# Optimization experiments

Hardware: AMD Instinct MI355X
Metric: run time of the kernel (lower is better)

The kernel has to match this reference:

```python
import jax, jax.numpy as jnp
import numpy as np

N_WIN = 7  # winsize in PSF.forward
EMBED_DIM = 3
N_EMBED = 8192

def _box_sum(x, n=N_WIN):
    # sliding-window sum with zero padding == torch ZeroPad2d + unfold sum
    C = x.shape[1]
    k = jnp.ones((C, 1, n, n), x.dtype)
    return jax.lax.conv_general_dilated(
        x, k, (1, 1), [(n // 2, n // 2)] * 2,
        feature_group_count=C, dimension_numbers=('NCHW', 'OIHW', 'NCHW'))

def _patch_stats(x, n=N_WIN):
    # mean / unbiased var over the n*n window (zeros included, matching unfold of zero-padded input)
    N = n * n
    s1 = _box_sum(x, n)
    s2 = _box_sum(x * x, n)
    mean = s1 / N
    var = (s2 - s1 * s1 / N) / (N - 1)  # torch .var default unbiased=True
    return mean, var

def _patch_mv_norm(x, n=N_WIN):
    m, v = _patch_stats(x, n)
    return (x - m) / (jnp.sqrt(v) + 1e-8)

def _conv1x1(x, w, b):
    return jnp.einsum('oi,bihw->bohw', w, x) + b[None, :, None, None]

def _ln(x, g, b, eps=1e-5):
    m = x.mean(-1, keepdims=True)
    v = x.var(-1, keepdims=True)
    return (x - m) / jnp.sqrt(v + eps) * g + b

def _mlp(x, w1, b1, w2, b2):
    h = jax.nn.gelu(x @ w1.T + b1, approximate=True)  # GELU(approximate='tanh')
    return h @ w2.T + b2

def _psf(front, back, e_w, e_b, f_w, f_b, g_w, g_b, h_w, h_b):
    x_norm = _patch_mv_norm(front)
    y_mean, y_var = _patch_stats(back)
    x_adain = x_norm * jnp.sqrt(y_var) + y_mean  # patch_adain (no eps on y_std)
    EE = _conv1x1(x_adain, e_w, e_b)
    FF = _conv1x1(_patch_mv_norm(front), f_w, f_b)
    GG = _conv1x1(_patch_mv_norm(back), g_w, g_b)
    HH = _conv1x1(back, h_w, h_b)
    b, c, h, w = GG.shape
    FFf = FF.reshape(b, c, h * w)
    GGf = GG.reshape(b, c, h * w)
    F_n = jnp.sqrt((FFf * FFf).sum(1))
    G_n = jnp.sqrt((GGf * GGf).sum(1))
    S = (FFf * GGf).sum(1) / (F_n * G_n)          # [b, h*w] cosine similarity
    S_min = S.min(1, keepdims=True)
    S_max = S.max(1, keepdims=True)
    S_n = ((S - S_min) / (S_max - S_min)).reshape(b, 1, h, w)
    return S_n * EE + (1 - S_n) * HH

def reference(front, back, mask, bg_embed,
              mi_w1, mi_b1, mi_w2, mi_b2,
              q_w, k_w, v_w,
              mo_w1, mo_b1, mo_w2, mo_b2,
              n1_g, n1_b, n2_g, n2_b,
              e_w, e_b, f_w, f_b, g_w, g_b, h_w, h_b,
              fuse_w, fuse_b):
    fused = _psf(front, back, e_w, e_b, f_w, f_b, g_w, g_b, h_w, h_b)  # [B,3,H,W]
    B, C, H, W = front.shape
    x = front.reshape(B, C, H * W).transpose(0, 2, 1)   # [B, HW, 3] pixel tokens
    x = _mlp(x, mi_w1, mi_b1, mi_w2, mi_b2)             # mlp_in: 3 -> 6 -> embed_dim
    x = _ln(x, n1_g, n1_b)                              # norm1
    ctx = bg_embed.T                                    # [n_embed, embed_dim] codebook as context
    q = x @ q_w.T                                       # [B, HW, d]
    k = ctx @ k_w.T                                     # [n_embed, d]
    v = ctx @ v_w.T                                     # [n_embed, d]
    scale = q.shape[-1] ** (-0.5)
    attn = jax.nn.softmax(jnp.einsum('bld,nd->bln', q, k) * scale, axis=-1)
    x = jnp.einsum('bln,nd->bld', attn, v)              # [B, HW, d]
    x = _mlp(x, mo_w1, mo_b1, mo_w2, mo_b2)             # mlp_out: d -> 6 -> 3
    x = _ln(x, n2_g, n2_b)                              # norm2
    attn_img = x.transpose(0, 2, 1).reshape(B, 3, H, W)
    out = _conv1x1(jnp.concatenate([attn_img, fused], 1), fuse_w, fuse_b)  # fuse: 6 -> 3
    return out

def setup_inputs() -> dict:
    key = jax.random.key(0)
    ks = jax.random.split(key, 32)
    B, H, W = 2, 96, 96
    d = EMBED_DIM
    n = lambda k, s: jax.random.normal(k, s, dtype=jnp.float32)
    inp = {
        'front': n(ks[0], (B, 3, H, W)),
        'back':  n(ks[1], (B, 3, H, W)),
        'mask':  jax.random.uniform(ks[2], (B, 1, H, W), dtype=jnp.float32),
        'bg_embed': n(ks[3], (d, N_EMBED)),
        'mi_w1': n(ks[4], (6, 3)) * 0.5, 'mi_b1': jnp.zeros((6,)),
        'mi_w2': n(ks[5], (d, 6)) * 0.5, 'mi_b2': jnp.zeros((d,)),
        'q_w': n(ks[6], (d, d)) * 0.5,
        'k_w': n(ks[7], (d, d)) * 0.5,
        'v_w': n(ks[8], (d, d)) * 0.5,
        'mo_w1': n(ks[9], (6, d)) * 0.5, 'mo_b1': jnp.zeros((6,)),
        'mo_w2': n(ks[10], (3, 6)) * 0.5, 'mo_b2': jnp.zeros((3,)),
        'n1_g': jnp.ones((d,)), 'n1_b': jnp.zeros((d,)),
        'n2_g': jnp.ones((3,)), 'n2_b': jnp.zeros((3,)),
        'e_w': n(ks[11], (3, 3)) * 0.3, 'e_b': jnp.zeros((3,)),
        'f_w': n(ks[12], (3, 3)) * 0.3, 'f_b': jnp.zeros((3,)),
        'g_w': n(ks[13], (3, 3)) * 0.3, 'g_b': jnp.zeros((3,)),
        'h_w': n(ks[14], (3, 3)) * 0.3, 'h_b': jnp.zeros((3,)),
        'fuse_w': n(ks[15], (3, 6)) * 0.3, 'fuse_b': jnp.zeros((3,)),
    }
    return inp
```

## Files before the change

kernel.cpp:

```cpp
#include <hip/hip_runtime.h>
#include <math.h>

#define HW    9216
#define NPIX  18432
#define NKEY  8192

#define OFF_QPK  0
#define OFF_KPK  (OFF_QPK + NPIX*8)
#define OFF_VT   (OFF_KPK + NKEY*8)
#define OFF_EEHS (OFF_VT + NKEY*4)
#define OFF_MM   (OFF_EEHS + NPIX*8)
#define OFF_PART (OFF_MM + 576)

#if __has_builtin(__builtin_amdgcn_exp2f)
#define EXP2(x) __builtin_amdgcn_exp2f(x)
#else
#define EXP2(x) exp2f(x)
#endif

typedef float f32x4 __attribute__((ext_vector_type(4)));
typedef short bf16x8 __attribute__((ext_vector_type(8)));
typedef unsigned u32x4 __attribute__((ext_vector_type(4)));

__device__ __forceinline__ unsigned bf16rne(float x){
    unsigned b = __builtin_bit_cast(unsigned, x);
    return (b + 0x7FFFu + ((b >> 16) & 1u)) >> 16;
}
__device__ __forceinline__ float bf16tof(unsigned h){
    return __builtin_bit_cast(float, h << 16);
}

__device__ __forceinline__ float gelu_tanh(float x){
    float u = 0.7978845608028654f*(x + 0.044715f*x*x*x);
    return 0.5f*x*(1.0f + tanhf(u));
}

__global__ __launch_bounds__(256) void k1_prep(
    const float* __restrict__ front, const float* __restrict__ back,
    const float* __restrict__ bg,
    const float* __restrict__ k_w,  const float* __restrict__ v_w,
    const float* __restrict__ mi_w1, const float* __restrict__ mi_b1,
    const float* __restrict__ mi_w2, const float* __restrict__ mi_b2,
    const float* __restrict__ q_w,
    const float* __restrict__ n1_g, const float* __restrict__ n1_b,
    const float* __restrict__ e_w,  const float* __restrict__ e_b,
    const float* __restrict__ f_w,  const float* __restrict__ f_b,
    const float* __restrict__ g_w,  const float* __restrict__ g_b,
    const float* __restrict__ h_w,  const float* __restrict__ h_b,
    float* __restrict__ ws)
{
    float* ws_qpk  = ws + OFF_QPK;
    float* ws_kpk  = ws + OFF_KPK;
    float* ws_eehs = ws + OFF_EEHS;
    float* ws_mm   = ws + OFF_MM;

    __shared__ float lds[6][484];

    int tid = threadIdx.x;
    int bid = blockIdx.x;
    int img = bid / 36;
    int t   = bid % 36;
    int ty  = (t / 6) * 16;
    int tx  = (t % 6) * 16;

    if (bid < 32){
        int key = bid*256 + tid;
        float c0=bg[key], c1=bg[NKEY+key], c2=bg[2*NKEY+key];
        float kv3[3], vv3[3];
        #pragma unroll
        for (int i=0;i<3;i++){
            kv3[i] = k_w[i*3+0]*c0 + k_w[i*3+1]*c1 + k_w[i*3+2]*c2;
            vv3[i] = v_w[i*3+0]*c0 + v_w[i*3+1]*c1 + v_w[i*3+2]*c2;
        }
        unsigned kh[3], kl[3];
        #pragma unroll
        for (int i=0;i<3;i++){
            kh[i] = bf16rne(kv3[i]);
            kl[i] = bf16rne(kv3[i] - bf16tof(kh[i]));
        }
        unsigned u[8];
        u[0] = kh[0] | (kh[1]<<16);
        u[1] = kh[2] | (kl[0]<<16);
        u[2] = kl[1] | (kl[2]<<16);
        u[3] = kh[0] | (kh[1]<<16);
        u[4] = kh[2]; u[5]=0; u[6]=0; u[7]=0;
        f32x4* kp4 = (f32x4*)ws_kpk;
        kp4[(size_t)key*2+0] = __builtin_bit_cast(f32x4, *(const u32x4*)&u[0]);
        kp4[(size_t)key*2+1] = __builtin_bit_cast(f32x4, *(const u32x4*)&u[4]);
        ((f32x4*)(ws + OFF_VT))[key] = (f32x4){vv3[0], vv3[1], vv3[2], 0.0f};
    }

    const float* fbase = front + img*3*HW;
    const float* bbase = back  + img*3*HW;

    for (int i = tid; i < 484; i += 256){
        int hy = i / 22, hx = i - hy*22;
        int gy = ty + hy - 3, gx = tx + hx - 3;
        bool ok = ((unsigned)gy < 96u) && ((unsigned)gx < 96u);
        int off = gy*96 + gx;
        #pragma unroll
        for (int c=0;c<3;c++){
            lds[c  ][i] = ok ? fbase[c*HW+off] : 0.0f;
            lds[3+c][i] = ok ? bbase[c*HW+off] : 0.0f;
        }
    }
    __syncthreads();

    int ly = tid / 16, lx = tid - ly*16;
    int y  = ty + ly,  x  = tx + lx;
    int pos = y*96 + x;
    int pix = img*HW + pos;

    float s1f[3]={0,0,0}, s2f[3]={0,0,0}, s1b[3]={0,0,0}, s2b[3]={0,0,0};
    #pragma unroll
    for (int dy=0; dy<7; ++dy){
        int rb = (ly+dy)*22 + lx;
        #pragma unroll
        for (int dx=0; dx<7; ++dx){
            #pragma unroll
            for (int c=0;c<3;c++){
                float fv = lds[c  ][rb+dx];
                float bv = lds[3+c][rb+dx];
                s1f[c]+=fv; s2f[c]+=fv*fv;
                s1b[c]+=bv; s2b[c]+=bv*bv;
            }
        }
    }

    int ctr = (ly+3)*22 + (lx+3);
    float xnf[3], adain[3], bn[3], bval[3], fctr[3];
    #pragma unroll
    for (int c=0;c<3;c++){
        float mf = s1f[c]*(1.0f/49.0f);
        float vf = (s2f[c] - s1f[c]*s1f[c]*(1.0f/49.0f))*(1.0f/48.0f);
        float fv = lds[c][ctr];
        fctr[c] = fv;
        xnf[c] = (fv - mf)/(sqrtf(vf)+1e-8f);

        float mb = s1b[c]*(1.0f/49.0f);
        float vb = (s2b[c] - s1b[c]*s1b[c]*(1.0f/49.0f))*(1.0f/48.0f);
        float bb = lds[3+c][ctr];
        bval[c]  = bb;
        float stdb = sqrtf(vb);
        adain[c] = xnf[c]*stdb + mb;
        bn[c]    = (bb - mb)/(stdb + 1e-8f);
    }

    float EE[3], FF[3], GG[3], HHv[3];
    #pragma unroll
    for (int i=0;i<3;i++){
        EE[i]  = e_w[i*3+0]*adain[0] + e_w[i*3+1]*adain[1] + e_w[i*3+2]*adain[2] + e_b[i];
        FF[i]  = f_w[i*3+0]*xnf[0]   + f_w[i*3+1]*xnf[1]   + f_w[i*3+2]*xnf[2]   + f_b[i];
        GG[i]  = g_w[i*3+0]*bn[0]    + g_w[i*3+1]*bn[1]    + g_w[i*3+2]*bn[2]    + g_b[i];
        HHv[i] = h_w[i*3+0]*bval[0]  + h_w[i*3+1]*bval[1]  + h_w[i*3+2]*bval[2]  + h_b[i];
    }
    float num = FF[0]*GG[0]+FF[1]*GG[1]+FF[2]*GG[2];
    float fn  = sqrtf(FF[0]*FF[0]+FF[1]*FF[1]+FF[2]*FF[2]);
    float gn  = sqrtf(GG[0]*GG[0]+GG[1]*GG[1]+GG[2]*GG[2]);
    float S   = num/(fn*gn);

    float4* eehs4 = (float4*)ws_eehs;
    eehs4[pix*2+0] = make_float4(EE[0],EE[1],EE[2],S);
    eehs4[pix*2+1] = make_float4(HHv[0],HHv[1],HHv[2],0.0f);

    float mn = S, mx = S;
    #pragma unroll
    for (int off=32; off>0; off>>=1){
        mn = fminf(mn, __shfl_xor(mn, off));
        mx = fmaxf(mx, __shfl_xor(mx, off));
    }
    if ((tid & 63) == 0){
        int entry = bid*4 + (tid>>6);
        ws_mm[entry*2+0]=mn; ws_mm[entry*2+1]=mx;
    }

    float xt0 = fctr[0], xt1 = fctr[1], xt2 = fctr[2];
    float h6[6];
    #pragma unroll
    for (int i=0;i<6;i++){
        float a = mi_w1[i*3+0]*xt0 + mi_w1[i*3+1]*xt1 + mi_w1[i*3+2]*xt2 + mi_b1[i];
        h6[i] = gelu_tanh(a);
    }
    float x2[3];
    #pragma unroll
    for (int i=0;i<3;i++){
        float a = mi_b2[i];
        #pragma unroll
        for (int k=0;k<6;k++) a += mi_w2[i*6+k]*h6[k];
        x2[i]=a;
    }
    float m  = (x2[0]+x2[1]+x2[2])*(1.0f/3.0f);
    float d0 = x2[0]-m, d1 = x2[1]-m, d2 = x2[2]-m;
    float var = (d0*d0+d1*d1+d2*d2)*(1.0f/3.0f);
    float inv = 1.0f/sqrtf(var+1e-5f);
    float xn0 = d0*inv*n1_g[0]+n1_b[0];
    float xn1 = d1*inv*n1_g[1]+n1_b[1];
    float xn2 = d2*inv*n1_g[2]+n1_b[2];
    const float qs = 0.5773502691896258f * 1.4426950408889634f;
    float qv[3];
    qv[0] = (q_w[0]*xn0 + q_w[1]*xn1 + q_w[2]*xn2)*qs;
    qv[1] = (q_w[3]*xn0 + q_w[4]*xn1 + q_w[5]*xn2)*qs;
    qv[2] = (q_w[6]*xn0 + q_w[7]*xn1 + q_w[8]*xn2)*qs;

    unsigned qh[3], ql[3];
    #pragma unroll
    for (int i=0;i<3;i++){
        qh[i] = bf16rne(qv[i]);
        ql[i] = bf16rne(qv[i] - bf16tof(qh[i]));
    }
    unsigned u[8];
    u[0] = qh[0] | (qh[1]<<16);
    u[1] = qh[2] | (qh[0]<<16);
    u[2] = qh[1] | (qh[2]<<16);
    u[3] = ql[0] | (ql[1]<<16);
    u[4] = ql[2]; u[5]=0; u[6]=0; u[7]=0;
    f32x4* qp4 = (f32x4*)ws_qpk;
    qp4[(size_t)pix*2+0] = __builtin_bit_cast(f32x4, *(const u32x4*)&u[0]);
    qp4[(size_t)pix*2+1] = __builtin_bit_cast(f32x4, *(const u32x4*)&u[4]);
}

#define RED4(vv, mm) { vv.x += __shfl_xor(vv.x,mm); vv.y += __shfl_xor(vv.y,mm); \
                       vv.z += __shfl_xor(vv.z,mm); vv.w += __shfl_xor(vv.w,mm); }

__global__ __launch_bounds__(256) void k2_attn(const float* __restrict__ ws)
{
    const f32x4* qpk = (const f32x4*)(ws + OFF_QPK);
    const f32x4* kpk = (const f32x4*)(ws + OFF_KPK);
    const f32x4* vt  = (const f32x4*)(ws + OFF_VT);
    f32x4* part      = (f32x4*)(ws + OFF_PART);

    __shared__ f32x4 lkp[512];
    __shared__ f32x4 lv[256];

    int tid  = threadIdx.x;
    int bid  = blockIdx.x;
    int kq   = bid & 7;
    int qg   = bid >> 3;
    int wave = tid >> 6, lane = tid & 63;
    int qtile = qg*4 + wave;
    int g = lane >> 4, col = lane & 15;

    bf16x8 afrag = {0,0,0,0,0,0,0,0};
    if (g < 2)
        afrag = __builtin_bit_cast(bf16x8, qpk[(size_t)(qtile*16 + col)*2 + g]);

    f32x4 s_ = {0,0,0,0}, a0_ = {0,0,0,0}, a1_ = {0,0,0,0}, a2_ = {0,0,0,0};

    const f32x4* kpbase = kpk + ((size_t)kq*1024)*2;
    const f32x4* vbase  = vt + kq*1024;

    for (int chunk=0; chunk<4; ++chunk){
        for (int i=tid; i<512; i+=256) lkp[i] = kpbase[chunk*512 + i];
        if (tid < 256)             lv[tid] = vbase[chunk*256 + tid];
        __syncthreads();
        #pragma unroll 4
        for (int st=0; st<16; ++st){
            bf16x8 bfrag = {0,0,0,0,0,0,0,0};
            if (g < 2)
                bfrag = __builtin_bit_cast(bf16x8, lkp[(st*16+col)*2 + g]);
            f32x4 S = __builtin_amdgcn_mfma_f32_16x16x32_bf16(afrag, bfrag, (f32x4){0,0,0,0}, 0, 0, 0);
            f32x4 v = lv[st*16+col];
            f32x4 p;
            p.x = EXP2(S.x); p.y = EXP2(S.y); p.z = EXP2(S.z); p.w = EXP2(S.w);
            s_  += p;
            a0_ += p * v.x;
            a1_ += p * v.y;
            a2_ += p * v.z;
        }
        __syncthreads();
    }

    RED4(s_, 8) RED4(a0_, 8) RED4(a1_, 8) RED4(a2_, 8)
    RED4(s_, 4) RED4(a0_, 4) RED4(a1_, 4) RED4(a2_, 4)
    RED4(s_, 2) RED4(a0_, 2) RED4(a1_, 2) RED4(a2_, 2)
    RED4(s_, 1) RED4(a0_, 1) RED4(a1_, 1) RED4(a2_, 1)

    int qbase = qtile*16 + g*4;
    f32x4* dst = part + (size_t)kq*NPIX + qbase;
    if      (col==0) dst[0] = (f32x4){s_.x, a0_.x, a1_.x, a2_.x};
    else if (col==1) dst[1] = (f32x4){s_.y, a0_.y, a1_.y, a2_.y};
    else if (col==2) dst[2] = (f32x4){s_.z, a0_.z, a1_.z, a2_.z};
    else if (col==3) dst[3] = (f32x4){s_.w, a0_.w, a1_.w, a2_.w};
}

template<int NC_T>
__global__ __launch_bounds__(256) void k3_final(
    const float* __restrict__ ws,
    const float* __restrict__ mo_w1, const float* __restrict__ mo_b1,
    const float* __restrict__ mo_w2, const float* __restrict__ mo_b2,
    const float* __restrict__ n2_g,  const float* __restrict__ n2_b,
    const float* __restrict__ fuse_w,const float* __restrict__ fuse_b,
    float* __restrict__ out)
{
    const float* ws_eehs = ws + OFF_EEHS;
    const float* ws_mm   = ws + OFF_MM;
    const float* ws_part = ws + OFF_PART;

    int tid = threadIdx.x;
    int g   = tid >> 6;
    int lp  = tid & 63;
    int pixbase = blockIdx.x*64;
    int pix = pixbase + lp;
    int b   = (pix >= HW) ? 1 : 0;

    constexpr int CPG = NC_T/4;
    float s=0.0f, a0=0.0f, a1=0.0f, a2=0.0f;
    const f32x4* part4 = (const f32x4*)ws_part;
    #pragma unroll
    for (int c=g*CPG; c<(g+1)*CPG; ++c){
        f32x4 p = part4[(size_t)c*NPIX + pix];
        s+=p.x; a0+=p.y; a1+=p.z; a2+=p.w;
    }
    __shared__ f32x4 red[256];
    red[tid] = (f32x4){s,a0,a1,a2};

    __shared__ float wmn[4], wmx[4];
    float mn = INFINITY, mx = -INFINITY;
    if (tid < 144){
        mn = ws_mm[(b*144+tid)*2+0];
        mx = ws_mm[(b*144+tid)*2+1];
    }
    #pragma unroll
    for (int off=32; off>0; off>>=1){
        mn = fminf(mn, __shfl_xor(mn, off));
        mx = fmaxf(mx, __shfl_xor(mx, off));
    }
    if ((tid & 63) == 0){ wmn[tid>>6]=mn; wmx[tid>>6]=mx; }
    __syncthreads();

    if (tid < 64){
        mn = fminf(fminf(wmn[0],wmn[1]), fminf(wmn[2],wmn[3]));
        mx = fmaxf(fmaxf(wmx[0],wmx[1]), fmaxf(wmx[2],wmx[3]));

        f32x4 p0 = red[tid], p1 = red[64+tid], p2 = red[128+tid], p3 = red[192+tid];
        s  = p0.x+p1.x+p2.x+p3.x;
        a0 = p0.y+p1.y+p2.y+p3.y;
        a1 = p0.z+p1.z+p2.z+p3.z;
        a2 = p0.w+p1.w+p2.w+p3.w;
        float invs = 1.0f/s;
        float xa0 = a0*invs, xa1 = a1*invs, xa2 = a2*invs;

        float h6[6];
        #pragma unroll
        for (int i=0;i<6;i++){
            float a = mo_w1[i*3+0]*xa0 + mo_w1[i*3+1]*xa1 + mo_w1[i*3+2]*xa2 + mo_b1[i];
            h6[i] = gelu_tanh(a);
        }
        float y[3];
        #pragma unroll
        for (int i=0;i<3;i++){
            float a = mo_b2[i];
            #pragma unroll
            for (int k=0;k<6;k++) a += mo_w2[i*6+k]*h6[k];
            y[i]=a;
        }
        float m  = (y[0]+y[1]+y[2])*(1.0f/3.0f);
        float d0 = y[0]-m, d1 = y[1]-m, d2 = y[2]-m;
        float var = (d0*d0+d1*d1+d2*d2)*(1.0f/3.0f);
        float inv = 1.0f/sqrtf(var+1e-5f);
        float t0 = d0*inv*n2_g[0]+n2_b[0];
        float t1 = d1*inv*n2_g[1]+n2_b[1];
        float t2 = d2*inv*n2_g[2]+n2_b[2];

        float4 e  = ((const float4*)ws_eehs)[pix*2+0];
        float4 hh = ((const float4*)ws_eehs)[pix*2+1];
        float Sn = (e.w - mn)/(mx - mn);
        float f0 = Sn*e.x + (1.0f-Sn)*hh.x;
        float f1 = Sn*e.y + (1.0f-Sn)*hh.y;
        float f2 = Sn*e.z + (1.0f-Sn)*hh.z;

        int pos = pix - b*HW;
        #pragma unroll
        for (int o=0;o<3;o++){
            float val = fuse_b[o]
                      + fuse_w[o*6+0]*t0 + fuse_w[o*6+1]*t1 + fuse_w[o*6+2]*t2
                      + fuse_w[o*6+3]*f0 + fuse_w[o*6+4]*f1 + fuse_w[o*6+5]*f2;
            out[(b*3+o)*HW + pos] = val;
        }
    }
}

extern "C" void kernel_launch(void* const* d_in, const int* in_sizes, int n_in,
                              void* d_out, int out_size, void* d_ws, size_t ws_size,
                              hipStream_t stream) {
    const float* front  = (const float*)d_in[0];
    const float* back   = (const float*)d_in[1];
    const float* bg     = (const float*)d_in[3];
    const float* mi_w1  = (const float*)d_in[4];
    const float* mi_b1  = (const float*)d_in[5];
    const float* mi_w2  = (const float*)d_in[6];
    const float* mi_b2  = (const float*)d_in[7];
    const float* q_w    = (const float*)d_in[8];
    const float* k_w    = (const float*)d_in[9];
    const float* v_w    = (const float*)d_in[10];
    const float* mo_w1  = (const float*)d_in[11];
    const float* mo_b1  = (const float*)d_in[12];
    const float* mo_w2  = (const float*)d_in[13];
    const float* mo_b2  = (const float*)d_in[14];
    const float* n1_g   = (const float*)d_in[15];
    const float* n1_b   = (const float*)d_in[16];
    const float* n2_g   = (const float*)d_in[17];
    const float* n2_b   = (const float*)d_in[18];
    const float* e_w    = (const float*)d_in[19];
    const float* e_b    = (const float*)d_in[20];
    const float* f_w    = (const float*)d_in[21];
    const float* f_b    = (const float*)d_in[22];
    const float* g_w    = (const float*)d_in[23];
    const float* g_b    = (const float*)d_in[24];
    const float* h_w    = (const float*)d_in[25];
    const float* h_b    = (const float*)d_in[26];
    const float* fuse_w = (const float*)d_in[27];
    const float* fuse_b = (const float*)d_in[28];

    float* ws  = (float*)d_ws;
    float* out = (float*)d_out;

    k1_prep<<<dim3(72), 256, 0, stream>>>(
        front, back, bg, k_w, v_w, mi_w1, mi_b1, mi_w2, mi_b2, q_w,
        n1_g, n1_b, e_w, e_b, f_w, f_b, g_w, g_b, h_w, h_b, ws);

    k2_attn<<<dim3(2304), 256, 0, stream>>>(ws);

    k3_final<8><<<dim3(NPIX/64), 256, 0, stream>>>(
        ws, mo_w1, mo_b1, mo_w2, mo_b2, n2_g, n2_b, fuse_w, fuse_b, out);
}
```

Before: 52.73 us.

## Split prep kernel into smaller tiles with 4 threads per pixel

The prep kernel now uses 8x8 pixel tiles over 288 blocks instead of 16x16 tiles over 72 blocks, so far more of the GPU's compute units get work. Each pixel's 7x7 window sums are split by rows across four waves, and the partial sums are combined through shared memory before one wave finishes the per-pixel math. The aim is to shorten this under-parallelised stage. The cost is an extra barrier, a larger shared-memory reduction buffer, more halo loads per pixel, and three of four waves sitting idle during the epilogue.

```diff
diff --git a/kernel.cpp b/kernel.cpp
--- a/kernel.cpp
+++ b/kernel.cpp
@@ -54,14 +54,15 @@
     float* ws_eehs = ws + OFF_EEHS;
     float* ws_mm   = ws + OFF_MM;
 
-    __shared__ float lds[6][484];
+    __shared__ float lds[6][196];
+    __shared__ float red[12][256];
 
     int tid = threadIdx.x;
     int bid = blockIdx.x;
-    int img = bid / 36;
-    int t   = bid % 36;
-    int ty  = (t / 6) * 16;
-    int tx  = (t % 6) * 16;
+    int img = bid / 144;
+    int t   = bid % 144;
+    int ty  = (t / 12) * 8;
+    int tx  = (t % 12) * 8;
 
     if (bid < 32){
         int key = bid*256 + tid;
@@ -93,8 +94,8 @@
     const float* fbase = front + img*3*HW;
     const float* bbase = back  + img*3*HW;
 
-    for (int i = tid; i < 484; i += 256){
-        int hy = i / 22, hx = i - hy*22;
+    for (int i = tid; i < 196; i += 256){
+        int hy = i / 14, hx = i - hy*14;
         int gy = ty + hy - 3, gx = tx + hx - 3;
         bool ok = ((unsigned)gy < 96u) && ((unsigned)gx < 96u);
         int off = gy*96 + gx;
@@ -106,117 +107,142 @@
     }
     __syncthreads();
 
-    int ly = tid / 16, lx = tid - ly*16;
-    int y  = ty + ly,  x  = tx + lx;
-    int pos = y*96 + x;
-    int pix = img*HW + pos;
-
-    float s1f[3]={0,0,0}, s2f[3]={0,0,0}, s1b[3]={0,0,0}, s2b[3]={0,0,0};
-    #pragma unroll
-    for (int dy=0; dy<7; ++dy){
-        int rb = (ly+dy)*22 + lx;
-        #pragma unroll
-        for (int dx=0; dx<7; ++dx){
+    int p  = tid & 63;
+    int qd = tid >> 6;
+    int ly = p >> 3, lx = p & 7;
+
+    {
+        float s1f[3]={0,0,0}, s2f[3]={0,0,0}, s1b[3]={0,0,0}, s2b[3]={0,0,0};
+        int r0 = qd*2;
+        int nr = (qd < 3) ? 2 : 1;
+        for (int rr=0; rr<nr; ++rr){
+            int rb = (ly + r0 + rr)*14 + lx;
+            #pragma unroll
+            for (int dx=0; dx<7; ++dx){
+                #pragma unroll
+                for (int c=0;c<3;c++){
+                    float fv = lds[c  ][rb+dx];
+                    float bv = lds[3+c][rb+dx];
+                    s1f[c]+=fv; s2f[c]+=fv*fv;
+                    s1b[c]+=bv; s2b[c]+=bv*bv;
+                }
+            }
+        }
+        #pragma unroll
+        for (int c=0;c<3;c++){
+            red[c  ][tid] = s1f[c];
+            red[3+c][tid] = s2f[c];
+            red[6+c][tid] = s1b[c];
+            red[9+c][tid] = s2b[c];
+        }
+    }
+    __syncthreads();
+
+    if (tid < 64){
+        float s1f[3]={0,0,0}, s2f[3]={0,0,0}, s1b[3]={0,0,0}, s2b[3]={0,0,0};
+        #pragma unroll
+        for (int q2=0; q2<4; ++q2){
+            int src = p + q2*64;
             #pragma unroll
             for (int c=0;c<3;c++){
-                float fv = lds[c  ][rb+dx];
-                float bv = lds[3+c][rb+dx];
-                s1f[c]+=fv; s2f[c]+=fv*fv;
-                s1b[c]+=bv; s2b[c]+=bv*bv;
+                s1f[c] += red[c  ][src];
+                s2f[c] += red[3+c][src];
+                s1b[c] += red[6+c][src];
+                s2b[c] += red[9+c][src];
             }
         }
-    }
-
-    int ctr = (ly+3)*22 + (lx+3);
-    float xnf[3], adain[3], bn[3], bval[3], fctr[3];
-    #pragma unroll
-    for (int c=0;c<3;c++){
-        float mf = s1f[c]*(1.0f/49.0f);
-        float vf = (s2f[c] - s1f[c]*s1f[c]*(1.0f/49.0f))*(1.0f/48.0f);
-        float fv = lds[c][ctr];
-        fctr[c] = fv;
-        xnf[c] = (fv - mf)/(sqrtf(vf)+1e-8f);
-
-        float mb = s1b[c]*(1.0f/49.0f);
-        float vb = (s2b[c] - s1b[c]*s1b[c]*(1.0f/49.0f))*(1.0f/48.0f);
-        float bb = lds[3+c][ctr];
-        bval[c]  = bb;
-        float stdb = sqrtf(vb);
-        adain[c] = xnf[c]*stdb + mb;
-        bn[c]    = (bb - mb)/(stdb + 1e-8f);
-    }
-
-    float EE[3], FF[3], GG[3], HHv[3];
-    #pragma unroll
-    for (int i=0;i<3;i++){
-        EE[i]  = e_w[i*3+0]*adain[0] + e_w[i*3+1]*adain[1] + e_w[i*3+2]*adain[2] + e_b[i];
-        FF[i]  = f_w[i*3+0]*xnf[0]   + f_w[i*3+1]*xnf[1]   + f_w[i*3+2]*xnf[2]   + f_b[i];
-        GG[i]  = g_w[i*3+0]*bn[0]    + g_w[i*3+1]*bn[1]    + g_w[i*3+2]*bn[2]    + g_b[i];
-        HHv[i] = h_w[i*3+0]*bval[0]  + h_w[i*3+1]*bval[1]  + h_w[i*3+2]*bval[2]  + h_b[i];
-    }
-    float num = FF[0]*GG[0]+FF[1]*GG[1]+FF[2]*GG[2];
-    float fn  = sqrtf(FF[0]*FF[0]+FF[1]*FF[1]+FF[2]*FF[2]);
-    float gn  = sqrtf(GG[0]*GG[0]+GG[1]*GG[1]+GG[2]*GG[2]);
-    float S   = num/(fn*gn);
-
-    float4* eehs4 = (float4*)ws_eehs;
-    eehs4[pix*2+0] = make_float4(EE[0],EE[1],EE[2],S);
-    eehs4[pix*2+1] = make_float4(HHv[0],HHv[1],HHv[2],0.0f);
-
-    float mn = S, mx = S;
-    #pragma unroll
-    for (int off=32; off>0; off>>=1){
-        mn = fminf(mn, __shfl_xor(mn, off));
-        mx = fmaxf(mx, __shfl_xor(mx, off));
-    }
-    if ((tid & 63) == 0){
-        int entry = bid*4 + (tid>>6);
-        ws_mm[entry*2+0]=mn; ws_mm[entry*2+1]=mx;
-    }
-
-    float xt0 = fctr[0], xt1 = fctr[1], xt2 = fctr[2];
-    float h6[6];
-    #pragma unroll
-    for (int i=0;i<6;i++){
-        float a = mi_w1[i*3+0]*xt0 + mi_w1[i*3+1]*xt1 + mi_w1[i*3+2]*xt2 + mi_b1[i];
-        h6[i] = gelu_tanh(a);
-    }
-    float x2[3];
-    #pragma unroll
-    for (int i=0;i<3;i++){
-        float a = mi_b2[i];
-        #pragma unroll
-        for (int k=0;k<6;k++) a += mi_w2[i*6+k]*h6[k];
-        x2[i]=a;
-    }
-    float m  = (x2[0]+x2[1]+x2[2])*(1.0f/3.0f);
-    float d0 = x2[0]-m, d1 = x2[1]-m, d2 = x2[2]-m;
-    float var = (d0*d0+d1*d1+d2*d2)*(1.0f/3.0f);
-    float inv = 1.0f/sqrtf(var+1e-5f);
-    float xn0 = d0*inv*n1_g[0]+n1_b[0];
-    float xn1 = d1*inv*n1_g[1]+n1_b[1];
-    float xn2 = d2*inv*n1_g[2]+n1_b[2];
-    const float qs = 0.5773502691896258f * 1.4426950408889634f;
-    float qv[3];
-    qv[0] = (q_w[0]*xn0 + q_w[1]*xn1 + q_w[2]*xn2)*qs;
-    qv[1] = (q_w[3]*xn0 + q_w[4]*xn1 + q_w[5]*xn2)*qs;
-    qv[2] = (q_w[6]*xn0 + q_w[7]*xn1 + q_w[8]*xn2)*qs;
-
-    unsigned qh[3], ql[3];
-    #pragma unroll
-    for (int i=0;i<3;i++){
-        qh[i] = bf16rne(qv[i]);
-        ql[i] = bf16rne(qv[i] - bf16tof(qh[i]));
-    }
-    unsigned u[8];
-    u[0] = qh[0] | (qh[1]<<16);
-    u[1] = qh[2] | (qh[0]<<16);
-    u[2] = qh[1] | (qh[2]<<16);
-    u[3] = ql[0] | (ql[1]<<16);
-    u[4] = ql[2]; u[5]=0; u[6]=0; u[7]=0;
-    f32x4* qp4 = (f32x4*)ws_qpk;
-    qp4[(size_t)pix*2+0] = __builtin_bit_cast(f32x4, *(const u32x4*)&u[0]);
-    qp4[(size_t)pix*2+1] = __builtin_bit_cast(f32x4, *(const u32x4*)&u[4]);
+
+        int ctr = (ly+3)*14 + (lx+3);
+        int pos = (ty+ly)*96 + (tx+lx);
+        int pix = img*HW + pos;
+
+        float xnf[3], adain[3], bn[3], bval[3], fctr[3];
+        #pragma unroll
+        for (int c=0;c<3;c++){
+            float mf = s1f[c]*(1.0f/49.0f);
+            float vf = (s2f[c] - s1f[c]*s1f[c]*(1.0f/49.0f))*(1.0f/48.0f);
+            float fv = lds[c][ctr];
+            fctr[c] = fv;
+            xnf[c] = (fv - mf)/(sqrtf(vf)+1e-8f);
+
+            float mb = s1b[c]*(1.0f/49.0f);
+            float vb = (s2b[c] - s1b[c]*s1b[c]*(1.0f/49.0f))*(1.0f/48.0f);
+            float bb = lds[3+c][ctr];
+            bval[c]  = bb;
+            float stdb = sqrtf(vb);
+            adain[c] = xnf[c]*stdb + mb;
+            bn[c]    = (bb - mb)/(stdb + 1e-8f);
+        }
+
+        float EE[3], FF[3], GG[3], HHv[3];
+        #pragma unroll
+        for (int i=0;i<3;i++){
+            EE[i]  = e_w[i*3+0]*adain[0] + e_w[i*3+1]*adain[1] + e_w[i*3+2]*adain[2] + e_b[i];
+            FF[i]  = f_w[i*3+0]*xnf[0]   + f_w[i*3+1]*xnf[1]   + f_w[i*3+2]*xnf[2]   + f_b[i];
+            GG[i]  = g_w[i*3+0]*bn[0]    + g_w[i*3+1]*bn[1]    + g_w[i*3+2]*bn[2]    + g_b[i];
+            HHv[i] = h_w[i*3+0]*bval[0]  + h_w[i*3+1]*bval[1]  + h_w[i*3+2]*bval[2]  + h_b[i];
+        }
+        float num = FF[0]*GG[0]+FF[1]*GG[1]+FF[2]*GG[2];
+        float fn  = sqrtf(FF[0]*FF[0]+FF[1]*FF[1]+FF[2]*FF[2]);
+        float gn  = sqrtf(GG[0]*GG[0]+GG[1]*GG[1]+GG[2]*GG[2]);
+        float S   = num/(fn*gn);
+
+        float4* eehs4 = (float4*)ws_eehs;
+        eehs4[pix*2+0] = make_float4(EE[0],EE[1],EE[2],S);
+        eehs4[pix*2+1] = make_float4(HHv[0],HHv[1],HHv[2],0.0f);
+
+        float mn = S, mx = S;
+        #pragma unroll
+        for (int off=32; off>0; off>>=1){
+            mn = fminf(mn, __shfl_xor(mn, off));
+            mx = fmaxf(mx, __shfl_xor(mx, off));
+        }
+        if (p == 0){ ws_mm[bid*2+0]=mn; ws_mm[bid*2+1]=mx; }
+
+        float xt0 = fctr[0], xt1 = fctr[1], xt2 = fctr[2];
+        float h6[6];
+        #pragma unroll
+        for (int i=0;i<6;i++){
+            float a = mi_w1[i*3+0]*xt0 + mi_w1[i*3+1]*xt1 + mi_w1[i*3+2]*xt2 + mi_b1[i];
+            h6[i] = gelu_tanh(a);
+        }
+        float x2[3];
+        #pragma unroll
+        for (int i=0;i<3;i++){
+            float a = mi_b2[i];
+            #pragma unroll
+            for (int k=0;k<6;k++) a += mi_w2[i*6+k]*h6[k];
+            x2[i]=a;
+        }
+        float m  = (x2[0]+x2[1]+x2[2])*(1.0f/3.0f);
+        float d0 = x2[0]-m, d1 = x2[1]-m, d2 = x2[2]-m;
+        float var = (d0*d0+d1*d1+d2*d2)*(1.0f/3.0f);
+        float inv = 1.0f/sqrtf(var+1e-5f);
+        float xn0 = d0*inv*n1_g[0]+n1_b[0];
+        float xn1 = d1*inv*n1_g[1]+n1_b[1];
+        float xn2 = d2*inv*n1_g[2]+n1_b[2];
+        const float qs = 0.5773502691896258f * 1.4426950408889634f;
+        float qv[3];
+        qv[0] = (q_w[0]*xn0 + q_w[1]*xn1 + q_w[2]*xn2)*qs;
+        qv[1] = (q_w[3]*xn0 + q_w[4]*xn1 + q_w[5]*xn2)*qs;
+        qv[2] = (q_w[6]*xn0 + q_w[7]*xn1 + q_w[8]*xn2)*qs;
+
+        unsigned qh[3], ql[3];
+        #pragma unroll
+        for (int i=0;i<3;i++){
+            qh[i] = bf16rne(qv[i]);
+            ql[i] = bf16rne(qv[i] - bf16tof(qh[i]));
+        }
+        unsigned u[8];
+        u[0] = qh[0] | (qh[1]<<16);
+        u[1] = qh[2] | (qh[0]<<16);
+        u[2] = qh[1] | (qh[2]<<16);
+        u[3] = ql[0] | (ql[1]<<16);
+        u[4] = ql[2]; u[5]=0; u[6]=0; u[7]=0;
+        f32x4* qp4 = (f32x4*)ws_qpk;
+        qp4[(size_t)pix*2+0] = __builtin_bit_cast(f32x4, *(const u32x4*)&u[0]);
+        qp4[(size_t)pix*2+1] = __builtin_bit_cast(f32x4, *(const u32x4*)&u[4]);
+    }
 }
 
 #define RED4(vv, mm) { vv.x += __shfl_xor(vv.x,mm); vv.y += __shfl_xor(vv.y,mm); \
@@ -415,7 +441,7 @@
     float* ws  = (float*)d_ws;
     float* out = (float*)d_out;
 
-    k1_prep<<<dim3(72), 256, 0, stream>>>(
+    k1_prep<<<dim3(288), 256, 0, stream>>>(
         front, back, bg, k_w, v_w, mi_w1, mi_b1, mi_w2, mi_b2, q_w,
         n1_g, n1_b, e_w, e_b, f_w, f_b, g_w, g_b, h_w, h_b, ws);
 
```

New measurement: 50.15 us (median of 2 runs). 1.05x faster.
